# Optimization experiments

Hardware: AMD Instinct MI355X
Metric: run time of the kernel (lower is better)

## Reference

```python
import jax, jax.numpy as jnp
import numpy as np

B, H, SQ, SK, D = 2, 16, 2048, 2048, 128
P_DROP = 0.5


def setup_inputs() -> dict:
    key = jax.random.key(0)
    kq, kk, kv, km = jax.random.split(key, 4)
    query = jax.random.normal(kq, (B, H, SQ, D), dtype=jnp.float32)
    key_t = jax.random.normal(kk, (B, H, SK, D), dtype=jnp.float32)
    value = jax.random.normal(kv, (B, H, SK, D), dtype=jnp.float32)
    # deterministic Bernoulli(0.5) keep-mask standing in for dropout(p=0.5, train=True)
    dropout_mask = jax.random.randint(km, (B, H, SQ, SK), 0, 2, dtype=jnp.int32)
    return {"query": query, "key": key_t, "value": value, "dropout_mask": dropout_mask}


def reference(query, key, value, dropout_mask):
    d = query.shape[-1]
    # original: scaled_qk = qk.div(d ** -0.5)  ==  qk * sqrt(d)  (faithful to source)
    scale = jnp.asarray(d, query.dtype) ** 0.5
    qk = jnp.einsum("bhqd,bhkd->bhqk", query, key)  # [B,H,SQ,SK]
    scaled_qk = qk * scale
    keep_scale = jnp.asarray(1.0 / (1.0 - P_DROP), query.dtype)
    dropped = jnp.where(dropout_mask == 1, scaled_qk * keep_scale, jnp.zeros((), query.dtype))
    out = jnp.einsum("bhqk,bhkd->bhqd", dropped, value)  # [B,H,SQ,D]
    return out
```

## Files before the change

kernel.cpp:

```cpp
#include <hip/hip_runtime.h>
#include <hip/hip_bf16.h>

#define B_   2
#define H_   16
#define SQ_  2048
#define SK_  2048
#define D_   128

#define QT   128
#define KT   64
#define NITER (SK_/KT)

using bf16x8 = __attribute__((ext_vector_type(8))) __bf16;
using bf16x4 = __attribute__((ext_vector_type(4))) __bf16;
using f32x4  = __attribute__((ext_vector_type(4))) float;

#define MFMA16(a,b,c) __builtin_amdgcn_mfma_f32_16x16x32_bf16(a,b,c,0,0,0)

#define QK_PITCH 136
#define VT_PITCH 72
#define P_PITCH  72

#define KLDS_BYTES (KT  * QK_PITCH * 2)
#define VT_BYTES   (D_  * VT_PITCH * 2)
#define P_BYTES    (QT  * P_PITCH  * 2)
#define SMEM_BYTES (KLDS_BYTES + VT_BYTES + P_BYTES)

__global__ __launch_bounds__(256, 2)
void attn_drop_kernel(const float* __restrict__ Q,
                      const float* __restrict__ K,
                      const float* __restrict__ V,
                      const int*   __restrict__ M,
                      float* __restrict__ Out)
{
    __shared__ __align__(16) char smem[SMEM_BYTES];
    __bf16* Qs = (__bf16*)smem;
    __bf16* Ks = (__bf16*)smem;
    __bf16* Vt = (__bf16*)(smem + KLDS_BYTES);
    __bf16* Ps = (__bf16*)(smem + KLDS_BYTES + VT_BYTES);

    const int tid  = threadIdx.x;
    const int wave = tid >> 6;
    const int lane = tid & 63;
    const int quad = lane >> 4;
    const int ln   = lane & 15;

    const int bh = blockIdx.x >> 4;
    const int qb = blockIdx.x & 15;

    const float* qptr = Q + ((size_t)bh*SQ_ + (size_t)qb*QT) * D_;
    const float* kptr = K + (size_t)bh*SK_*D_;
    const float* vptr = V + (size_t)bh*SK_*D_;
    const int*   mptr = M + (size_t)bh*SQ_*SK_ + (size_t)qb*QT*SK_;
    float*       optr = Out + ((size_t)bh*SQ_ + (size_t)qb*QT) * D_;

    const int c = tid & 31;
    const int g = tid >> 5;

    {
        const float4* src = (const float4*)qptr;
        #pragma unroll
        for (int p = 0; p < 16; ++p) {
            int r = g + 8*p;
            float4 v = src[r*32 + c];
            bf16x4 h = { (__bf16)v.x, (__bf16)v.y, (__bf16)v.z, (__bf16)v.w };
            *(bf16x4*)&Qs[r*QK_PITCH + 4*c] = h;
        }
    }
    __syncthreads();

    bf16x8 qf[2][4];
    #pragma unroll
    for (int rt = 0; rt < 2; ++rt)
        #pragma unroll
        for (int s = 0; s < 4; ++s)
            qf[rt][s] = *(const bf16x8*)&Qs[(32*wave + 16*rt + ln)*QK_PITCH + 32*s + 8*quad];
    __syncthreads();

    f32x4 Oacc[2][8];
    #pragma unroll
    for (int rt = 0; rt < 2; ++rt)
        #pragma unroll
        for (int dt = 0; dt < 8; ++dt)
            Oacc[rt][dt] = (f32x4){0.f, 0.f, 0.f, 0.f};

    for (int kt = 0; kt < NITER; ++kt) {
        {
            const float4* src = (const float4*)(kptr + (size_t)kt*KT*D_);
            #pragma unroll
            for (int p = 0; p < 8; ++p) {
                int r = g + 8*p;
                float4 v = src[r*32 + c];
                bf16x4 h = { (__bf16)v.x, (__bf16)v.y, (__bf16)v.z, (__bf16)v.w };
                *(bf16x4*)&Ks[r*QK_PITCH + 4*c] = h;
            }
        }
        {
            const float4* src = (const float4*)(vptr + (size_t)kt*KT*D_);
            float4 fv[8];
            #pragma unroll
            for (int i = 0; i < 8; ++i) fv[i] = src[(8*g + i)*32 + c];
            const float* ff = (const float*)fv;
            #pragma unroll
            for (int j = 0; j < 4; ++j) {
                bf16x8 row = { (__bf16)ff[0*4+j], (__bf16)ff[1*4+j],
                               (__bf16)ff[2*4+j], (__bf16)ff[3*4+j],
                               (__bf16)ff[4*4+j], (__bf16)ff[5*4+j],
                               (__bf16)ff[6*4+j], (__bf16)ff[7*4+j] };
                *(bf16x8*)&Vt[(4*c + j)*VT_PITCH + 8*g] = row;
            }
        }
        __syncthreads();

        f32x4 S[2][4];
        #pragma unroll
        for (int rt = 0; rt < 2; ++rt)
            #pragma unroll
            for (int ct = 0; ct < 4; ++ct)
                S[rt][ct] = (f32x4){0.f, 0.f, 0.f, 0.f};

        #pragma unroll
        for (int s = 0; s < 4; ++s) {
            #pragma unroll
            for (int ct = 0; ct < 4; ++ct) {
                bf16x8 kf = *(const bf16x8*)&Ks[(16*ct + ln)*QK_PITCH + 32*s + 8*quad];
                S[0][ct] = MFMA16(qf[0][s], kf, S[0][ct]);
                S[1][ct] = MFMA16(qf[1][s], kf, S[1][ct]);
            }
        }

        #pragma unroll
        for (int rt = 0; rt < 2; ++rt) {
            #pragma unroll
            for (int ct = 0; ct < 4; ++ct) {
                int row0 = 32*wave + 16*rt + 4*quad;
                int col  = kt*KT + 16*ct + ln;
                #pragma unroll
                for (int r = 0; r < 4; ++r) {
                    int m = mptr[(size_t)(row0 + r)*SK_ + col];
                    float pv = m ? S[rt][ct][r] : 0.0f;
                    Ps[(row0 + r)*P_PITCH + 16*ct + ln] = (__bf16)pv;
                }
            }
        }

        #pragma unroll
        for (int ks = 0; ks < 2; ++ks) {
            bf16x8 pf0 = *(const bf16x8*)&Ps[(32*wave +      ln)*P_PITCH + 32*ks + 8*quad];
            bf16x8 pf1 = *(const bf16x8*)&Ps[(32*wave + 16 + ln)*P_PITCH + 32*ks + 8*quad];
            #pragma unroll
            for (int dt = 0; dt < 8; ++dt) {
                bf16x8 vf = *(const bf16x8*)&Vt[(16*dt + ln)*VT_PITCH + 32*ks + 8*quad];
                Oacc[0][dt] = MFMA16(pf0, vf, Oacc[0][dt]);
                Oacc[1][dt] = MFMA16(pf1, vf, Oacc[1][dt]);
            }
        }
        __syncthreads();
    }

    const float SCALE = 22.62741699796952f;
    #pragma unroll
    for (int rt = 0; rt < 2; ++rt) {
        #pragma unroll
        for (int dt = 0; dt < 8; ++dt) {
            int row0 = 32*wave + 16*rt + 4*quad;
            #pragma unroll
            for (int r = 0; r < 4; ++r)
                optr[(size_t)(row0 + r)*D_ + 16*dt + ln] = Oacc[rt][dt][r] * SCALE;
        }
    }
}

extern "C" void kernel_launch(void* const* d_in, const int* in_sizes, int n_in,
                              void* d_out, int out_size, void* d_ws, size_t ws_size,
                              hipStream_t stream) {
    (void)in_sizes; (void)n_in; (void)d_ws; (void)ws_size; (void)out_size;
    const float* Q = (const float*)d_in[0];
    const float* K = (const float*)d_in[1];
    const float* V = (const float*)d_in[2];
    const int*   M = (const int*)d_in[3];
    float* Out = (float*)d_out;

    dim3 grid(B_ * H_ * (SQ_ / QT));
    attn_drop_kernel<<<grid, 256, 0, stream>>>(Q, K, V, M, Out);
}
```

Before: 799.8 us.

## Precast Q/K/V to bf16 in workspace and prefetch tiles through registers

Adds two pre-kernels that convert Q and K to bf16 and write V transposed in bf16 into the workspace, so the attention kernel no longer converts fp32 inside every block. The main loop now prefetches the next K/V tile into registers while computing the current one. The dropout mask is read with vectorized nontemporal loads and applied when the P fragments are loaded, instead of through scalar per-element loads. This removes 16x redundant fp32 K/V reads and conversions and widens the mask traffic, at the cost of two extra launches and workspace round-trips.

```diff
diff --git a/kernel.cpp b/kernel.cpp
--- a/kernel.cpp
+++ b/kernel.cpp
@@ -6,7 +6,6 @@
 #define SQ_  2048
 #define SK_  2048
 #define D_   128
-
 #define QT   128
 #define KT   64
 #define NITER (SK_/KT)
@@ -14,30 +13,91 @@
 using bf16x8 = __attribute__((ext_vector_type(8))) __bf16;
 using bf16x4 = __attribute__((ext_vector_type(4))) __bf16;
 using f32x4  = __attribute__((ext_vector_type(4))) float;
+using i32x4  = __attribute__((ext_vector_type(4))) int;
 
 #define MFMA16(a,b,c) __builtin_amdgcn_mfma_f32_16x16x32_bf16(a,b,c,0,0,0)
 
-#define QK_PITCH 136
-#define VT_PITCH 72
-#define P_PITCH  72
-
-#define KLDS_BYTES (KT  * QK_PITCH * 2)
-#define VT_BYTES   (D_  * VT_PITCH * 2)
-#define P_BYTES    (QT  * P_PITCH  * 2)
-#define SMEM_BYTES (KLDS_BYTES + VT_BYTES + P_BYTES)
+#define QOFF 0u
+#define KOFF (1u<<25)
+#define VOFF (1u<<26)
+
+#define KPITCH 136
+#define VPITCH 72
+#define PPITCH 72
+#define KB_BYTES (KT*KPITCH*2)
+#define VB_BYTES (D_*VPITCH*2)
+#define PB_BYTES (QT*PPITCH*2)
+
+__device__ __forceinline__ bf16x8 mask8(bf16x8 p, i32x4 a, i32x4 b) {
+    bf16x8 r;
+    r[0] = a[0] ? p[0] : (__bf16)0.0f;
+    r[1] = a[1] ? p[1] : (__bf16)0.0f;
+    r[2] = a[2] ? p[2] : (__bf16)0.0f;
+    r[3] = a[3] ? p[3] : (__bf16)0.0f;
+    r[4] = b[0] ? p[4] : (__bf16)0.0f;
+    r[5] = b[1] ? p[5] : (__bf16)0.0f;
+    r[6] = b[2] ? p[6] : (__bf16)0.0f;
+    r[7] = b[3] ? p[7] : (__bf16)0.0f;
+    return r;
+}
+
+__global__ __launch_bounds__(256)
+void cast_qk(const float* __restrict__ Q, const float* __restrict__ K,
+             char* __restrict__ ws)
+{
+    const size_t idx = (size_t)blockIdx.x * 256 + threadIdx.x;
+    const float4* q4 = (const float4*)Q;
+    const float4* k4 = (const float4*)K;
+    bf16x4* qd = (bf16x4*)(ws + QOFF);
+    bf16x4* kd = (bf16x4*)(ws + KOFF);
+    #pragma unroll
+    for (int i = 0; i < 4; ++i) {
+        size_t f = idx + (size_t)i * 524288;
+        float4 a = q4[f];
+        qd[f] = (bf16x4){ (__bf16)a.x, (__bf16)a.y, (__bf16)a.z, (__bf16)a.w };
+        float4 b = k4[f];
+        kd[f] = (bf16x4){ (__bf16)b.x, (__bf16)b.y, (__bf16)b.z, (__bf16)b.w };
+    }
+}
+
+__global__ __launch_bounds__(256)
+void transpose_v(const float* __restrict__ V, char* __restrict__ ws)
+{
+    __shared__ __align__(16) __bf16 vlds[64 * 132];
+    const int blk = blockIdx.x;
+    const int t   = threadIdx.x;
+
+    const float4* src = (const float4*)(V + (size_t)blk * KT * D_);
+    #pragma unroll
+    for (int i = 0; i < 8; ++i) {
+        int f = t + 256 * i;
+        float4 v = src[f];
+        int row = f >> 5, col = f & 31;
+        *(bf16x4*)&vlds[row * 132 + col * 4] =
+            (bf16x4){ (__bf16)v.x, (__bf16)v.y, (__bf16)v.z, (__bf16)v.w };
+    }
+    __syncthreads();
+
+    __bf16* dst = (__bf16*)(ws + VOFF) + (size_t)blk * (D_ * KT);
+    const int d = t >> 1, h = t & 1;
+    #pragma unroll
+    for (int c = 0; c < 4; ++c) {
+        bf16x8 frag;
+        #pragma unroll
+        for (int j = 0; j < 8; ++j) frag[j] = vlds[(h * 32 + c * 8 + j) * 132 + d];
+        *(bf16x8*)&dst[d * KT + h * 32 + c * 8] = frag;
+    }
+}
 
 __global__ __launch_bounds__(256, 2)
-void attn_drop_kernel(const float* __restrict__ Q,
-                      const float* __restrict__ K,
-                      const float* __restrict__ V,
-                      const int*   __restrict__ M,
+void attn_drop_kernel(const char* __restrict__ ws,
+                      const int*  __restrict__ M,
                       float* __restrict__ Out)
 {
-    __shared__ __align__(16) char smem[SMEM_BYTES];
-    __bf16* Qs = (__bf16*)smem;
-    __bf16* Ks = (__bf16*)smem;
-    __bf16* Vt = (__bf16*)(smem + KLDS_BYTES);
-    __bf16* Ps = (__bf16*)(smem + KLDS_BYTES + VT_BYTES);
+    __shared__ __align__(16) char smem[KB_BYTES + VB_BYTES + PB_BYTES];
+    __bf16* Kb = (__bf16*)smem;
+    __bf16* Vb = (__bf16*)(smem + KB_BYTES);
+    __bf16* Pb = (__bf16*)(smem + KB_BYTES + VB_BYTES);
 
     const int tid  = threadIdx.x;
     const int wave = tid >> 6;
@@ -48,34 +108,18 @@
     const int bh = blockIdx.x >> 4;
     const int qb = blockIdx.x & 15;
 
-    const float* qptr = Q + ((size_t)bh*SQ_ + (size_t)qb*QT) * D_;
-    const float* kptr = K + (size_t)bh*SK_*D_;
-    const float* vptr = V + (size_t)bh*SK_*D_;
-    const int*   mptr = M + (size_t)bh*SQ_*SK_ + (size_t)qb*QT*SK_;
-    float*       optr = Out + ((size_t)bh*SQ_ + (size_t)qb*QT) * D_;
-
-    const int c = tid & 31;
-    const int g = tid >> 5;
-
-    {
-        const float4* src = (const float4*)qptr;
-        #pragma unroll
-        for (int p = 0; p < 16; ++p) {
-            int r = g + 8*p;
-            float4 v = src[r*32 + c];
-            bf16x4 h = { (__bf16)v.x, (__bf16)v.y, (__bf16)v.z, (__bf16)v.w };
-            *(bf16x4*)&Qs[r*QK_PITCH + 4*c] = h;
-        }
-    }
-    __syncthreads();
+    const __bf16* Qbf = (const __bf16*)(ws + QOFF);
+    const __bf16* Kbf = (const __bf16*)(ws + KOFF);
+    const __bf16* Vtt = (const __bf16*)(ws + VOFF);
+    const int* mbase = M + ((size_t)bh * SQ_ + (size_t)qb * QT) * SK_;
+    float* optr = Out + ((size_t)bh * SQ_ + (size_t)qb * QT) * D_;
 
     bf16x8 qf[2][4];
     #pragma unroll
     for (int rt = 0; rt < 2; ++rt)
         #pragma unroll
         for (int s = 0; s < 4; ++s)
-            qf[rt][s] = *(const bf16x8*)&Qs[(32*wave + 16*rt + ln)*QK_PITCH + 32*s + 8*quad];
-    __syncthreads();
+            qf[rt][s] = *(const bf16x8*)&Qbf[((size_t)bh*SQ_ + qb*QT + 32*wave + 16*rt + ln)*D_ + 32*s + 8*quad];
 
     f32x4 Oacc[2][8];
     #pragma unroll
@@ -84,33 +128,47 @@
         for (int dt = 0; dt < 8; ++dt)
             Oacc[rt][dt] = (f32x4){0.f, 0.f, 0.f, 0.f};
 
+    bf16x8 kreg[4], vreg[4];
+    {
+        const __bf16* kp = Kbf + ((size_t)bh*SK_ + 0*KT) * D_;
+        const __bf16* vp = Vtt + (size_t)(bh*32 + 0) * (D_*KT);
+        #pragma unroll
+        for (int j = 0; j < 4; ++j) {
+            kreg[j] = *(const bf16x8*)&kp[j*2048 + tid*8];
+            vreg[j] = *(const bf16x8*)&vp[j*2048 + tid*8];
+        }
+    }
+
+    #pragma unroll 1
     for (int kt = 0; kt < NITER; ++kt) {
+        __syncthreads();
+        #pragma unroll
+        for (int j = 0; j < 4; ++j) {
+            *(bf16x8*)&Kb[(16*j + (tid>>4))*KPITCH + (tid&15)*8] = kreg[j];
+            *(bf16x8*)&Vb[(32*j + (tid>>3))*VPITCH + (tid&7)*8]  = vreg[j];
+        }
+        __syncthreads();
+
+        i32x4 mreg[2][2][2];
+        #pragma unroll
+        for (int rt = 0; rt < 2; ++rt)
+            #pragma unroll
+            for (int ks = 0; ks < 2; ++ks)
+                #pragma unroll
+                for (int i = 0; i < 2; ++i)
+                    mreg[rt][ks][i] = __builtin_nontemporal_load(
+                        (const i32x4*)&mbase[(size_t)(32*wave + 16*rt + ln)*SK_ + kt*KT + 32*ks + 8*quad + 4*i]);
+
         {
-            const float4* src = (const float4*)(kptr + (size_t)kt*KT*D_);
-            #pragma unroll
-            for (int p = 0; p < 8; ++p) {
-                int r = g + 8*p;
-                float4 v = src[r*32 + c];
-                bf16x4 h = { (__bf16)v.x, (__bf16)v.y, (__bf16)v.z, (__bf16)v.w };
-                *(bf16x4*)&Ks[r*QK_PITCH + 4*c] = h;
-            }
-        }
-        {
-            const float4* src = (const float4*)(vptr + (size_t)kt*KT*D_);
-            float4 fv[8];
-            #pragma unroll
-            for (int i = 0; i < 8; ++i) fv[i] = src[(8*g + i)*32 + c];
-            const float* ff = (const float*)fv;
+            const int nkt = (kt + 1 < NITER) ? kt + 1 : NITER - 1;
+            const __bf16* kp = Kbf + ((size_t)bh*SK_ + nkt*KT) * D_;
+            const __bf16* vp = Vtt + (size_t)(bh*32 + nkt) * (D_*KT);
             #pragma unroll
             for (int j = 0; j < 4; ++j) {
-                bf16x8 row = { (__bf16)ff[0*4+j], (__bf16)ff[1*4+j],
-                               (__bf16)ff[2*4+j], (__bf16)ff[3*4+j],
-                               (__bf16)ff[4*4+j], (__bf16)ff[5*4+j],
-                               (__bf16)ff[6*4+j], (__bf16)ff[7*4+j] };
-                *(bf16x8*)&Vt[(4*c + j)*VT_PITCH + 8*g] = row;
-            }
-        }
-        __syncthreads();
+                kreg[j] = *(const bf16x8*)&kp[j*2048 + tid*8];
+                vreg[j] = *(const bf16x8*)&vp[j*2048 + tid*8];
+            }
+        }
 
         f32x4 S[2][4];
         #pragma unroll
@@ -120,47 +178,42 @@
                 S[rt][ct] = (f32x4){0.f, 0.f, 0.f, 0.f};
 
         #pragma unroll
-        for (int s = 0; s < 4; ++s) {
+        for (int s = 0; s < 4; ++s)
             #pragma unroll
             for (int ct = 0; ct < 4; ++ct) {
-                bf16x8 kf = *(const bf16x8*)&Ks[(16*ct + ln)*QK_PITCH + 32*s + 8*quad];
+                bf16x8 kf = *(const bf16x8*)&Kb[(16*ct + ln)*KPITCH + 32*s + 8*quad];
                 S[0][ct] = MFMA16(qf[0][s], kf, S[0][ct]);
                 S[1][ct] = MFMA16(qf[1][s], kf, S[1][ct]);
             }
-        }
-
-        #pragma unroll
-        for (int rt = 0; rt < 2; ++rt) {
+
+        #pragma unroll
+        for (int rt = 0; rt < 2; ++rt)
             #pragma unroll
             for (int ct = 0; ct < 4; ++ct) {
                 int row0 = 32*wave + 16*rt + 4*quad;
-                int col  = kt*KT + 16*ct + ln;
                 #pragma unroll
-                for (int r = 0; r < 4; ++r) {
-                    int m = mptr[(size_t)(row0 + r)*SK_ + col];
-                    float pv = m ? S[rt][ct][r] : 0.0f;
-                    Ps[(row0 + r)*P_PITCH + 16*ct + ln] = (__bf16)pv;
-                }
-            }
-        }
+                for (int r = 0; r < 4; ++r)
+                    Pb[(row0 + r)*PPITCH + 16*ct + ln] = (__bf16)S[rt][ct][r];
+            }
 
         #pragma unroll
         for (int ks = 0; ks < 2; ++ks) {
-            bf16x8 pf0 = *(const bf16x8*)&Ps[(32*wave +      ln)*P_PITCH + 32*ks + 8*quad];
-            bf16x8 pf1 = *(const bf16x8*)&Ps[(32*wave + 16 + ln)*P_PITCH + 32*ks + 8*quad];
+            bf16x8 pf0 = mask8(*(const bf16x8*)&Pb[(32*wave +      ln)*PPITCH + 32*ks + 8*quad],
+                               mreg[0][ks][0], mreg[0][ks][1]);
+            bf16x8 pf1 = mask8(*(const bf16x8*)&Pb[(32*wave + 16 + ln)*PPITCH + 32*ks + 8*quad],
+                               mreg[1][ks][0], mreg[1][ks][1]);
             #pragma unroll
             for (int dt = 0; dt < 8; ++dt) {
-                bf16x8 vf = *(const bf16x8*)&Vt[(16*dt + ln)*VT_PITCH + 32*ks + 8*quad];
+                bf16x8 vf = *(const bf16x8*)&Vb[(16*dt + ln)*VPITCH + 32*ks + 8*quad];
                 Oacc[0][dt] = MFMA16(pf0, vf, Oacc[0][dt]);
                 Oacc[1][dt] = MFMA16(pf1, vf, Oacc[1][dt]);
             }
         }
-        __syncthreads();
     }
 
     const float SCALE = 22.62741699796952f;
     #pragma unroll
-    for (int rt = 0; rt < 2; ++rt) {
+    for (int rt = 0; rt < 2; ++rt)
         #pragma unroll
         for (int dt = 0; dt < 8; ++dt) {
             int row0 = 32*wave + 16*rt + 4*quad;
@@ -168,19 +221,20 @@
             for (int r = 0; r < 4; ++r)
                 optr[(size_t)(row0 + r)*D_ + 16*dt + ln] = Oacc[rt][dt][r] * SCALE;
         }
-    }
 }
 
 extern "C" void kernel_launch(void* const* d_in, const int* in_sizes, int n_in,
                               void* d_out, int out_size, void* d_ws, size_t ws_size,
                               hipStream_t stream) {
-    (void)in_sizes; (void)n_in; (void)d_ws; (void)ws_size; (void)out_size;
+    (void)in_sizes; (void)n_in; (void)ws_size; (void)out_size;
     const float* Q = (const float*)d_in[0];
     const float* K = (const float*)d_in[1];
     const float* V = (const float*)d_in[2];
     const int*   M = (const int*)d_in[3];
     float* Out = (float*)d_out;
-
-    dim3 grid(B_ * H_ * (SQ_ / QT));
-    attn_drop_kernel<<<grid, 256, 0, stream>>>(Q, K, V, M, Out);
-}
+    char* ws = (char*)d_ws;
+
+    cast_qk<<<dim3(2048), 256, 0, stream>>>(Q, K, ws);
+    transpose_v<<<dim3(B_*H_*(SK_/KT)), 256, 0, stream>>>(V, ws);
+    attn_drop_kernel<<<dim3(B_*H_*(SQ_/QT)), 256, 0, stream>>>(ws, M, Out);
+}
```

Measured after the change: 803.2 us. Within noise of the previous version (+0.4%).
